# Optimization experiments

Hardware: AMD Instinct MI355X
Metric: run time of the kernel (lower is better)

Reference implementation:

```python
import jax, jax.numpy as jnp
import numpy as np

B, C, D, DE, NH = 4, 4, 96, 96, 3
NS, HIN, TOTAL_Z, PZ = 12, 128, 64, 32
WZ = WH = WW = 4
N_WIN_TOK = WZ * WH * WW  # 64 tokens per 3D window


def _rel_index():
    # standard Swin-3D relative position index, (N, N) into a (7*7*7, NH) table
    c = np.stack(np.meshgrid(np.arange(WZ), np.arange(WH), np.arange(WW), indexing='ij')).reshape(3, -1)
    r = (c[:, :, None] - c[:, None, :]).transpose(1, 2, 0)
    r += np.array([WZ - 1, WH - 1, WW - 1])
    r[:, :, 0] *= (2 * WH - 1) * (2 * WW - 1)
    r[:, :, 1] *= (2 * WW - 1)
    return jnp.asarray(r.sum(-1))

REL_IDX = _rel_index()


def layernorm(x, g, b, eps=1e-5):
    m = x.mean(-1, keepdims=True)
    v = x.var(-1, keepdims=True)
    return (x - m) * jax.lax.rsqrt(v + eps) * g + b


def groupnorm(x, g, b, groups=8, eps=1e-5):
    Bb, Cc, Z, H, W = x.shape
    xr = x.reshape(Bb, groups, Cc // groups, Z, H, W)
    m = xr.mean((2, 3, 4, 5), keepdims=True)
    v = xr.var((2, 3, 4, 5), keepdims=True)
    xr = (xr - m) * jax.lax.rsqrt(v + eps)
    return xr.reshape(Bb, Cc, Z, H, W) * g[None, :, None, None, None] + b[None, :, None, None, None]


def conv3d(x, w, b):
    y = jax.lax.conv_general_dilated(x, w, (1, 1, 1), 'SAME', dimension_numbers=('NCDHW', 'OIDHW', 'NCDHW'))
    return y + b[None, :, None, None, None]


def z_interp(x, pos, out_z):
    """Linear interp along z. x:(B,C,S,H,W), pos:(S,) sorted float positions.
    Matches the torch loop: clamp below first / above last, weight=0.5 on ties."""
    S = x.shape[2]
    zq = jnp.arange(out_z, dtype=jnp.float32)
    right = jnp.searchsorted(pos, zq, side='left')  # first i with pos[i] >= z
    left = jnp.clip(right - 1, 0, S - 1)
    rc = jnp.clip(right, 0, S - 1)
    lp, rp = pos[left], pos[rc]
    d = rp - lp
    w = jnp.where(d > 0, (zq - lp) / jnp.where(d > 0, d, 1.0), 0.5)
    w = w[None, None, :, None, None]
    return (1.0 - w) * x[:, :, left] + w * x[:, :, rc]


def reference(sparse_obs, encoder_feat, pe_w, pe_b, pe_g, pe_beta, enc_w, enc_b, ln_g, ln_b,
              qkv_w, qkv_b, attn_w, attn_b, rpb, ref_w1, ref_b1, gn1_g, gn1_b,
              ref_w2, ref_b2, gn2_g, gn2_b, rec_w, rec_b, sparse_indices):
    Bb, Cc, Sz, H, W = sparse_obs.shape
    pos = sparse_indices.astype(jnp.float32)
    # --- skip connection: z-interp baseline at full resolution ---
    baseline = z_interp(sparse_obs, pos, TOTAL_Z)  # (B,C,64,128,128)
    # --- sparse patch embed: conv (1,4,4) stride (1,4,4) + LN ---
    xr = sparse_obs.reshape(Bb, Cc, Sz, H // 4, 4, W // 4, 4)
    f = jnp.einsum('bczhpwq,dcpq->bdzhw', xr, pe_w) + pe_b[None, :, None, None, None]
    f = layernorm(f.transpose(0, 2, 3, 4, 1), pe_g, pe_beta).transpose(0, 4, 1, 2, 3)
    # position-aware z interpolation into patch space (patch_size_z = 2)
    f = z_interp(f, pos / 2.0, PZ)  # (B,D,32,32,32)
    # --- encoder 1x1x1 projection + fuse ---
    enc = jnp.einsum('bczhw,dc->bdzhw', encoder_feat, enc_w) + enc_b[None, :, None, None, None]
    f = f + enc
    # --- 3D window attention with relative position bias (pre-norm, residual) ---
    nz = PZ // WZ
    x = f.transpose(0, 2, 3, 4, 1)  # (B,Z,H,W,D)
    xw = x.reshape(Bb, nz, WZ, nz, WH, nz, WW, D).transpose(0, 1, 3, 5, 2, 4, 6, 7).reshape(-1, N_WIN_TOK, D)
    sc = xw
    xn = layernorm(xw, ln_g, ln_b)
    dh = D // NH
    qkv = (xn @ qkv_w.T + qkv_b).reshape(-1, N_WIN_TOK, 3, NH, dh).transpose(2, 0, 3, 1, 4)
    q, k, v = qkv[0], qkv[1], qkv[2]  # (nWin*B, NH, N, dh)
    att = jnp.einsum('whnd,whmd->whnm', q * (dh ** -0.5), k)
    att = att + rpb[REL_IDX].transpose(2, 0, 1)[None]  # (.., NH, N, N)
    att = jax.nn.softmax(att, axis=-1)
    o = jnp.einsum('whnm,whmd->whnd', att, v).transpose(0, 2, 1, 3).reshape(-1, N_WIN_TOK, D)
    xw = sc + (o @ attn_w.T + attn_b)
    x = xw.reshape(Bb, nz, nz, nz, WZ, WH, WW, D).transpose(0, 1, 4, 2, 5, 3, 6, 7).reshape(Bb, PZ, PZ, PZ, D)
    f = x.transpose(0, 4, 1, 2, 3)
    f = jax.nn.gelu(groupnorm(conv3d(f, ref_w1, ref_b1), gn1_g, gn1_b), approximate=False)
    f = jax.nn.gelu(groupnorm(conv3d(f, ref_w2, ref_b2), gn2_g, gn2_b), approximate=False)
    # --- patch recovery: ConvTranspose3d kernel=stride=(2,4,4) as einsum+reshape ---
    delta = jnp.einsum('bizhw,iodef->bozdhewf', f, rec_w).reshape(Bb, Cc, PZ * 2, PZ * 4, PZ * 4)
    delta = delta + rec_b[None, :, None, None, None]
    return baseline + delta


def setup_inputs():
    key = jax.random.key(0)
    ks = jax.random.split(key, 16)
    n = lambda i, shape: jax.random.normal(ks[i], shape, dtype=jnp.float32) * 0.02
    return {
        'sparse_obs': jax.random.normal(ks[0], (B, C, NS, HIN, HIN), dtype=jnp.float32),
        'encoder_feat': jax.random.normal(ks[1], (B, DE, PZ, PZ, PZ), dtype=jnp.float32),
        'pe_w': n(2, (D, C, 4, 4)), 'pe_b': jnp.zeros((D,)), 'pe_g': jnp.ones((D,)), 'pe_beta': jnp.zeros((D,)),
        'enc_w': n(3, (D, DE)), 'enc_b': jnp.zeros((D,)),
        'ln_g': jnp.ones((D,)), 'ln_b': jnp.zeros((D,)),
        'qkv_w': n(4, (3 * D, D)), 'qkv_b': jnp.zeros((3 * D,)),
        'attn_w': n(5, (D, D)), 'attn_b': jnp.zeros((D,)),
        'rpb': n(6, ((2 * WZ - 1) * (2 * WH - 1) * (2 * WW - 1), NH)),
        'ref_w1': n(7, (D, D, 3, 3, 3)), 'ref_b1': jnp.zeros((D,)), 'gn1_g': jnp.ones((D,)), 'gn1_b': jnp.zeros((D,)),
        'ref_w2': n(8, (D, D, 3, 3, 3)), 'ref_b2': jnp.zeros((D,)), 'gn2_g': jnp.ones((D,)), 'gn2_b': jnp.zeros((D,)),
        'rec_w': n(9, (D, C, 2, 4, 4)), 'rec_b': jnp.zeros((C,)),
        'sparse_indices': jnp.asarray(np.round(np.linspace(0, 63, 12)).astype(np.int64)),
    }
```

## Files before the change

kernel.cpp:

```cpp
#include <hip/hip_runtime.h>
#include <math.h>

typedef __attribute__((ext_vector_type(8))) short short8v;
typedef __attribute__((ext_vector_type(4))) float float4v;

__device__ inline unsigned short f2bf(float f) {
  unsigned u = __float_as_uint(f);
  return (unsigned short)((u + 0x7fff + ((u >> 16) & 1)) >> 16);
}
__device__ inline unsigned pk2(float a, float b) {
  return (unsigned)f2bf(a) | ((unsigned)f2bf(b) << 16);
}
__device__ inline float bfl(unsigned u) { return __uint_as_float(u << 16); }
__device__ inline float bfh(unsigned u) { return __uint_as_float(u & 0xffff0000u); }
__device__ inline float bfs(short s) { return __uint_as_float(((unsigned)(unsigned short)s) << 16); }

__global__ __launch_bounds__(96) void k_tables(const int* __restrict__ sidx, int* __restrict__ T) {
  __shared__ float pos[12];
  int t = threadIdx.x;
  if (t < 12) pos[t] = (float)sidx[t];
  __syncthreads();
  if (t < 64) {
    float zq = (float)t;
    int r = 0;
    while (r < 12 && pos[r] < zq) r++;
    int l = r - 1; if (l < 0) l = 0; if (l > 11) l = 11;
    int rc = r; if (rc > 11) rc = 11;
    float lp = pos[l], rp = pos[rc], d = rp - lp;
    float w = d > 0.f ? (zq - lp) / d : 0.5f;
    T[t] = l; T[64 + t] = rc; ((float*)T)[128 + t] = w;
  } else {
    int zq = t - 64;
    float zqf = (float)zq;
    int r = 0;
    while (r < 12 && pos[r] * 0.5f < zqf) r++;
    int l = r - 1; if (l < 0) l = 0; if (l > 11) l = 11;
    int rc = r; if (rc > 11) rc = 11;
    float lp = pos[l] * 0.5f, rp = pos[rc] * 0.5f, d = rp - lp;
    float w = d > 0.f ? (zqf - lp) / d : 0.5f;
    T[192 + zq] = l; T[224 + zq] = rc; ((float*)T)[256 + zq] = w;
  }
}

__global__ __launch_bounds__(256) void k_wcv(const float* __restrict__ w, short* __restrict__ Wt) {
  int id = blockIdx.x * 256 + threadIdx.x;
  if (id >= 248832) return;
  float v = w[id];
  int o = id / 2592; int rem = id % 2592; int i = rem / 27; int tap = rem % 27;
  Wt[(tap * 96 + o) * 96 + i] = (short)f2bf(v);
}

__global__ __launch_bounds__(256) void k_cvt(const float* __restrict__ src, short* __restrict__ dst, int n) {
  int id = blockIdx.x * 256 + threadIdx.x;
  if (id < n) dst[id] = (short)f2bf(src[id]);
}

__global__ __launch_bounds__(256) void k_wrt(const float* __restrict__ src, short* __restrict__ dst) {
  int id = blockIdx.x * 256 + threadIdx.x;
  if (id >= 12288) return;
  int i = id >> 7, j = id & 127;
  dst[j * 96 + i] = (short)f2bf(src[id]);
}

__global__ __launch_bounds__(256) void k_bias(const float* __restrict__ rpb, float* __restrict__ Bt) {
  int id = blockIdx.x * 256 + threadIdx.x;
  if (id >= 12288) return;
  int head = id >> 12, rem = id & 4095, n = rem >> 6, m = rem & 63;
  int dz = (n >> 4) - (m >> 4), dh = ((n >> 2) & 3) - ((m >> 2) & 3), dw = (n & 3) - (m & 3);
  Bt[id] = rpb[((dz + 3) * 49 + (dh + 3) * 7 + (dw + 3)) * 3 + head];
}

__global__ __launch_bounds__(256) void k_pe(const float* __restrict__ sp, const short* __restrict__ Wpe,
    const float* __restrict__ pb, const float* __restrict__ pg, const float* __restrict__ pbeta,
    float* __restrict__ f1) {
  int x = blockIdx.x;
  int b = x / 384, z = (x / 32) % 12, h = x % 32;
  __shared__ short sB[32][72];
  __shared__ float sF[32][97];
  __shared__ float sM[32], sR[32];
  int tid = threadIdx.x;
  for (int id = tid; id < 2048; id += 256) {
    int c = id >> 9, p = (id >> 7) & 3, col = id & 127;
    float v = sp[(((b * 4 + c) * 12 + z) * 128 + h * 4 + p) * 128 + col];
    sB[col >> 2][c * 16 + p * 4 + (col & 3)] = (short)f2bf(v);
  }
  __syncthreads();
  int w = tid >> 6, l = tid & 63, lo = l & 15, ig = l >> 4;
  int nt = w & 1, mbase = (w >> 1) * 3;
  short8v bfrag[2];
  #pragma unroll
  for (int kc = 0; kc < 2; kc++)
    bfrag[kc] = *(const short8v*)&sB[nt * 16 + lo][kc * 32 + ig * 8];
  #pragma unroll
  for (int mi = 0; mi < 3; mi++) {
    int m = mbase + mi;
    float4v acc = (float4v){0.f, 0.f, 0.f, 0.f};
    #pragma unroll
    for (int kc = 0; kc < 2; kc++) {
      short8v a = *(const short8v*)(Wpe + (size_t)(m * 16 + lo) * 64 + kc * 32 + ig * 8);
      acc = __builtin_amdgcn_mfma_f32_16x16x32_bf16(a, bfrag[kc], acc, 0, 0, 0);
    }
    int wcoord = nt * 16 + lo;
    #pragma unroll
    for (int r = 0; r < 4; r++) {
      int d = m * 16 + ig * 4 + r;
      sF[wcoord][d] = acc[r] + pb[d];
    }
  }
  __syncthreads();
  if (tid < 32) {
    int wv = tid;
    float s = 0.f, ss = 0.f;
    for (int d = 0; d < 96; d++) { float v = sF[wv][d]; s += v; ss += v * v; }
    float m = s * (1.f / 96.f);
    float var = ss * (1.f / 96.f) - m * m;
    sM[wv] = m; sR[wv] = rsqrtf(var + 1e-5f);
  }
  __syncthreads();
  for (int id = tid; id < 3072; id += 256) {
    int d = id >> 5, wv = id & 31;
    float v = (sF[wv][d] - sM[wv]) * sR[wv] * pg[d] + pbeta[d];
    f1[(((b * 96 + d) * 12 + z) * 32 + h) * 32 + wv] = v;
  }
}

__global__ __launch_bounds__(256) void k_ie(const float* __restrict__ f1, const float* __restrict__ ef,
    const short* __restrict__ Wenc, const float* __restrict__ eb, const int* __restrict__ T,
    unsigned* __restrict__ Xg) {
  int x = blockIdx.x;
  int b = x >> 9, chunk = x & 511;
  int v0 = chunk * 64;
  int z = v0 >> 10, rp = v0 & 1023;
  int zl = T[192 + z], zr = T[224 + z];
  float wt = ((const float*)T)[256 + z];
  __shared__ short sEb[64][104];
  int tid = threadIdx.x;
  for (int id = tid; id < 6144; id += 256) {
    int c = id >> 6, vs = id & 63;
    sEb[vs][c] = (short)f2bf(ef[(size_t)(b * 96 + c) * 32768 + v0 + vs]);
  }
  __syncthreads();
  int w = tid >> 6, l = tid & 63, lo = l & 15, ig = l >> 4;
  int vcol = w * 16 + lo;
  short8v bfrag[3];
  #pragma unroll
  for (int kc = 0; kc < 3; kc++)
    bfrag[kc] = *(const short8v*)&sEb[vcol][kc * 32 + ig * 8];
  float4v acc[6];
  #pragma unroll
  for (int m = 0; m < 6; m++) {
    acc[m] = (float4v){0.f, 0.f, 0.f, 0.f};
    #pragma unroll
    for (int kc = 0; kc < 3; kc++) {
      short8v a = *(const short8v*)(Wenc + (size_t)(m * 16 + lo) * 96 + kc * 32 + ig * 8);
      acc[m] = __builtin_amdgcn_mfma_f32_16x16x32_bf16(a, bfrag[kc], acc[m], 0, 0, 0);
    }
  }
  int zb = z >> 2, tz = z & 3;
  int h0 = (chunk & 15) * 2;
  int h = h0 + (vcol >> 5), wc = vcol & 31;
  int win = ((b * 8 + zb) * 8 + (h >> 2)) * 8 + (wc >> 2);
  int t = tz * 16 + (h & 3) * 4 + (wc & 3);
  size_t xbase = (size_t)(win * 64 + t) * 48;
  float wl = 1.f - wt;
  #pragma unroll
  for (int m = 0; m < 6; m++) {
    #pragma unroll
    for (int rr = 0; rr < 2; rr++) {
      int d0 = m * 16 + ig * 4 + rr * 2;
      const float* p1a = f1 + ((size_t)(b * 96 + d0) * 12 + zl) * 1024 + rp + vcol;
      const float* p2a = f1 + ((size_t)(b * 96 + d0) * 12 + zr) * 1024 + rp + vcol;
      const float* p1b = f1 + ((size_t)(b * 96 + d0 + 1) * 12 + zl) * 1024 + rp + vcol;
      const float* p2b = f1 + ((size_t)(b * 96 + d0 + 1) * 12 + zr) * 1024 + rp + vcol;
      float va = acc[m][rr * 2] + eb[d0] + wl * p1a[0] + wt * p2a[0];
      float vb = acc[m][rr * 2 + 1] + eb[d0 + 1] + wl * p1b[0] + wt * p2b[0];
      Xg[xbase + m * 8 + ig * 2 + rr] = pk2(va, vb);
    }
  }
}

__global__ __launch_bounds__(512) void k_qkv(const unsigned* __restrict__ Xg, const short* __restrict__ Wq,
    const float* __restrict__ qb, const float* __restrict__ lg, const float* __restrict__ lb,
    short* __restrict__ Qg, short* __restrict__ Kg, short* __restrict__ Vg) {
  int win = blockIdx.x;
  __shared__ short sX[64][104];
  __shared__ short sVt[96][72];
  __shared__ float sM[64], sRr[64];
  int tid = threadIdx.x;
  for (int id = tid; id < 3072; id += 512) {
    int row = id / 48, c2 = id % 48;
    *(unsigned*)&sX[row][c2 * 2] = Xg[(size_t)(win * 64 + row) * 48 + c2];
  }
  __syncthreads();
  {
    int token = tid >> 3, j = tid & 7;
    float s = 0.f, ss = 0.f;
    #pragma unroll
    for (int i = 0; i < 12; i++) {
      float v = bfs(sX[token][j * 12 + i]);
      s += v; ss += v * v;
    }
    s += __shfl_xor(s, 1); ss += __shfl_xor(ss, 1);
    s += __shfl_xor(s, 2); ss += __shfl_xor(ss, 2);
    s += __shfl_xor(s, 4); ss += __shfl_xor(ss, 4);
    if (j == 0) {
      float m = s * (1.f / 96.f);
      sM[token] = m;
      sRr[token] = rsqrtf(ss * (1.f / 96.f) - m * m + 1e-5f);
    }
  }
  __syncthreads();
  for (int id = tid; id < 3072; id += 512) {
    int row = id / 48, c2 = id % 48;
    unsigned u = *(unsigned*)&sX[row][c2 * 2];
    float m = sM[row], r = sRr[row];
    float v0 = (bfl(u) - m) * r * lg[2 * c2] + lb[2 * c2];
    float v1 = (bfh(u) - m) * r * lg[2 * c2 + 1] + lb[2 * c2 + 1];
    *(unsigned*)&sX[row][c2 * 2] = pk2(v0, v1);
  }
  __syncthreads();
  int w = tid >> 6, l = tid & 63, lo = l & 15, ig = l >> 4;
  int mt2 = w >> 1, nh = w & 1;
  short8v a[3];
  #pragma unroll
  for (int kc = 0; kc < 3; kc++)
    a[kc] = *(const short8v*)&sX[mt2 * 16 + lo][kc * 32 + ig * 8];
  for (int nt = nh * 9; nt < nh * 9 + 9; nt++) {
    float4v acc = (float4v){0.f, 0.f, 0.f, 0.f};
    #pragma unroll
    for (int kc = 0; kc < 3; kc++) {
      short8v bfr = *(const short8v*)(Wq + (size_t)(nt * 16 + lo) * 96 + kc * 32 + ig * 8);
      acc = __builtin_amdgcn_mfma_f32_16x16x32_bf16(a[kc], bfr, acc, 0, 0, 0);
    }
    int out = nt * 16 + lo;
    float bias = qb[out];
    if (nt < 6) {
      int head = out >> 5, c = out & 31;
      #pragma unroll
      for (int r = 0; r < 4; r++)
        Qg[((size_t)(win * 3 + head) * 64 + mt2 * 16 + ig * 4 + r) * 32 + c] =
            (short)f2bf((acc[r] + bias) * 0.17677669529663687f);
    } else if (nt < 12) {
      int o2 = out - 96, head = o2 >> 5, c = o2 & 31;
      #pragma unroll
      for (int r = 0; r < 4; r++)
        Kg[((size_t)(win * 3 + head) * 64 + mt2 * 16 + ig * 4 + r) * 32 + c] = (short)f2bf(acc[r] + bias);
    } else {
      int o2 = out - 192;
      #pragma unroll
      for (int r = 0; r < 4; r++)
        sVt[o2][mt2 * 16 + ig * 4 + r] = (short)f2bf(acc[r] + bias);
    }
  }
  __syncthreads();
  for (int id = tid; id < 768; id += 512) {
    int row = id >> 3, ch = id & 7;
    short8v v = *(short8v*)&sVt[row][ch * 8];
    *(short8v*)(Vg + ((size_t)(win * 3 + (row >> 5)) * 32 + (row & 31)) * 64 + ch * 8) = v;
  }
}

__global__ __launch_bounds__(256) void k_att2(const short* __restrict__ Qg, const short* __restrict__ Kg,
    const short* __restrict__ Vg, const float* __restrict__ Bt, short* __restrict__ Og) {
  __shared__ short Pl[4][64][72];
  int tid = threadIdx.x;
  int w = tid >> 6, l = tid & 63, lo = l & 15, ig = l >> 4;
  int gwh = blockIdx.x * 4 + w;
  int head = gwh % 3, win = gwh / 3;
  short8v q[4], k[4];
  #pragma unroll
  for (int mt = 0; mt < 4; mt++)
    q[mt] = *(const short8v*)(Qg + ((size_t)gwh * 64 + mt * 16 + lo) * 32 + ig * 8);
  #pragma unroll
  for (int nt = 0; nt < 4; nt++)
    k[nt] = *(const short8v*)(Kg + ((size_t)gwh * 64 + nt * 16 + lo) * 32 + ig * 8);
  float4v s[4][4];
  #pragma unroll
  for (int mt = 0; mt < 4; mt++)
    #pragma unroll
    for (int nt = 0; nt < 4; nt++)
      s[mt][nt] = __builtin_amdgcn_mfma_f32_16x16x32_bf16(q[mt], k[nt], (float4v){0.f, 0.f, 0.f, 0.f}, 0, 0, 0);
  const float* bt = Bt + head * 4096;
  #pragma unroll
  for (int mt = 0; mt < 4; mt++) {
    #pragma unroll
    for (int r = 0; r < 4; r++) {
      int tok = mt * 16 + ig * 4 + r;
      float v[4];
      float mx = -1e30f;
      #pragma unroll
      for (int nt = 0; nt < 4; nt++) {
        v[nt] = s[mt][nt][r] + bt[tok * 64 + nt * 16 + lo];
        mx = fmaxf(mx, v[nt]);
      }
      mx = fmaxf(mx, __shfl_xor(mx, 1));
      mx = fmaxf(mx, __shfl_xor(mx, 2));
      mx = fmaxf(mx, __shfl_xor(mx, 4));
      mx = fmaxf(mx, __shfl_xor(mx, 8));
      float sm = 0.f;
      #pragma unroll
      for (int nt = 0; nt < 4; nt++) { v[nt] = __expf(v[nt] - mx); sm += v[nt]; }
      sm += __shfl_xor(sm, 1);
      sm += __shfl_xor(sm, 2);
      sm += __shfl_xor(sm, 4);
      sm += __shfl_xor(sm, 8);
      float inv = 1.f / sm;
      #pragma unroll
      for (int nt = 0; nt < 4; nt++)
        Pl[w][tok][nt * 16 + lo] = (short)f2bf(v[nt] * inv);
    }
  }
  short8v pa[4][2], vb[2][2];
  #pragma unroll
  for (int mt = 0; mt < 4; mt++)
    #pragma unroll
    for (int kc = 0; kc < 2; kc++)
      pa[mt][kc] = *(const short8v*)&Pl[w][mt * 16 + lo][kc * 32 + ig * 8];
  #pragma unroll
  for (int ct = 0; ct < 2; ct++)
    #pragma unroll
    for (int kc = 0; kc < 2; kc++)
      vb[ct][kc] = *(const short8v*)(Vg + ((size_t)gwh * 32 + ct * 16 + lo) * 64 + kc * 32 + ig * 8);
  #pragma unroll
  for (int mt = 0; mt < 4; mt++)
    #pragma unroll
    for (int ct = 0; ct < 2; ct++) {
      float4v o = __builtin_amdgcn_mfma_f32_16x16x32_bf16(pa[mt][0], vb[ct][0], (float4v){0.f, 0.f, 0.f, 0.f}, 0, 0, 0);
      o = __builtin_amdgcn_mfma_f32_16x16x32_bf16(pa[mt][1], vb[ct][1], o, 0, 0, 0);
      #pragma unroll
      for (int r = 0; r < 4; r++)
        Og[((size_t)(win * 64 + mt * 16 + ig * 4 + r)) * 96 + head * 32 + ct * 16 + lo] = (short)f2bf(o[r]);
    }
}

__global__ __launch_bounds__(256) void k_proj(const short* __restrict__ Og, const unsigned* __restrict__ Xg,
    const short* __restrict__ Wa, const float* __restrict__ ab, short* __restrict__ Xt) {
  int win = blockIdx.x;
  __shared__ float sOut[64][100];
  int tid = threadIdx.x;
  int w = tid >> 6, l = tid & 63, lo = l & 15, ig = l >> 4;
  int mt = w;
  short8v a[3];
  #pragma unroll
  for (int kc = 0; kc < 3; kc++)
    a[kc] = *(const short8v*)(Og + ((size_t)(win * 64 + mt * 16 + lo)) * 96 + kc * 32 + ig * 8);
  #pragma unroll
  for (int nt = 0; nt < 6; nt++) {
    float4v acc = (float4v){0.f, 0.f, 0.f, 0.f};
    #pragma unroll
    for (int kc = 0; kc < 3; kc++) {
      short8v bfr = *(const short8v*)(Wa + (size_t)(nt * 16 + lo) * 96 + kc * 32 + ig * 8);
      acc = __builtin_amdgcn_mfma_f32_16x16x32_bf16(a[kc], bfr, acc, 0, 0, 0);
    }
    int out = nt * 16 + lo;
    float bias = ab[out];
    #pragma unroll
    for (int r = 0; r < 4; r++) {
      int tok = mt * 16 + ig * 4 + r;
      unsigned u = Xg[(size_t)(win * 64 + tok) * 48 + (out >> 1)];
      sOut[tok][out] = acc[r] + bias + ((out & 1) ? bfh(u) : bfl(u));
    }
  }
  __syncthreads();
  int b = win >> 9, zb = (win >> 6) & 7, hb = (win >> 3) & 7, wb = win & 7;
  for (int id = tid; id < 3072; id += 256) {
    int cc = id >> 10, rem = id & 1023, t = rem >> 4, ilp = rem & 15;
    int d0 = cc * 32 + ilp * 2;
    unsigned pk = pk2(sOut[t][d0], sOut[t][d0 + 1]);
    int tz = t >> 4, th = (t >> 2) & 3, tw = t & 3;
    size_t vox = (size_t)(zb * 4 + tz) * 1024 + (hb * 4 + th) * 32 + wb * 4 + tw;
    ((unsigned*)Xt)[((size_t)(b * 3 + cc) * 32768 + vox) * 16 + ilp] = pk;
  }
}

__global__ __launch_bounds__(512) void k_convM(const short* __restrict__ Xt,
    const short* __restrict__ Wt, const float* __restrict__ cb, float* __restrict__ y,
    float* __restrict__ stats) {
  int x = blockIdx.x;
  int b = x >> 6, zp = (x >> 2) & 15, hq = x & 3;
  int tid = threadIdx.x;
  int wvi = tid >> 6, l = tid & 63;
  int lo = l & 15, ig = l >> 4;
  int hp = wvi & 3, mh = wvi >> 2;
  __shared__ short Xl[54400];
  __shared__ float sG[16];
  if (tid < 16) sG[tid] = 0.f;
  float4v acc[3][2][2][2];
  #pragma unroll
  for (int mi = 0; mi < 3; mi++)
    #pragma unroll
    for (int zo = 0; zo < 2; zo++)
      #pragma unroll
      for (int hr = 0; hr < 2; hr++)
        #pragma unroll
        for (int n = 0; n < 2; n++) acc[mi][zo][hr][n] = (float4v){0.f, 0.f, 0.f, 0.f};

  for (int c = 0; c < 3; c++) {
    __syncthreads();
    for (int r = 0; r < 11; r++) {
      int id = tid + 512 * r;
      if (id < 5440) {
        int seg = id & 3, q = id >> 2;
        int zz = q / 340, rem = q - zz * 340;
        int hh = rem / 34, ww = rem - hh * 34;
        int gz = zp * 2 + zz - 1, gh = hq * 8 + hh - 1, gw = ww - 1;
        int4 val = {0, 0, 0, 0};
        if (gz >= 0 && gz < 32 && gh >= 0 && gh < 32 && gw >= 0 && gw < 32)
          val = *(const int4*)(Xt + ((size_t)((b * 3 + c) * 32768 + (gz << 10) + (gh << 5) + gw) * 32 + seg * 8));
        *(int4*)(&Xl[q * 40 + seg * 8]) = val;
      }
    }
    __syncthreads();
    for (int dh = 0; dh < 3; dh++) {
      for (int dwv = 0; dwv < 3; dwv++) {
        short8v bfr[4][2][2];
        #pragma unroll
        for (int zr = 0; zr < 4; zr++)
          #pragma unroll
          for (int hr = 0; hr < 2; hr++)
            #pragma unroll
            for (int n = 0; n < 2; n++) {
              int vox = (zr * 10 + hp * 2 + hr + dh) * 34 + n * 16 + lo + dwv;
              bfr[zr][hr][n] = *(const short8v*)&Xl[vox * 40 + ig * 8];
            }
        #pragma unroll
        for (int dz = 0; dz < 3; dz++) {
          int tap = dz * 9 + dh * 3 + dwv;
          #pragma unroll
          for (int mi = 0; mi < 3; mi++) {
            short8v wf = *(const short8v*)(Wt +
                ((size_t)(tap * 96 + (mh * 3 + mi) * 16 + lo)) * 96 + c * 32 + ig * 8);
            #pragma unroll
            for (int zo = 0; zo < 2; zo++)
              #pragma unroll
              for (int hr = 0; hr < 2; hr++)
                #pragma unroll
                for (int n = 0; n < 2; n++)
                  acc[mi][zo][hr][n] = __builtin_amdgcn_mfma_f32_16x16x32_bf16(wf, bfr[zo + dz][hr][n], acc[mi][zo][hr][n], 0, 0, 0);
          }
        }
      }
    }
  }
  #pragma unroll
  for (int mi = 0; mi < 3; mi++) {
    #pragma unroll
    for (int r = 0; r < 4; r++) {
      int o = (mh * 3 + mi) * 16 + ig * 4 + r;
      float cbo = cb[o];
      float s = 0.f, ss = 0.f;
      #pragma unroll
      for (int zo = 0; zo < 2; zo++)
        #pragma unroll
        for (int hr = 0; hr < 2; hr++)
          #pragma unroll
          for (int n = 0; n < 2; n++) {
            float v = acc[mi][zo][hr][n][r] + cbo;
            int z = zp * 2 + zo;
            int h = hq * 8 + hp * 2 + hr;
            int vcol = n * 16 + lo;
            y[((size_t)(b * 96 + o) << 15) + (z << 10) + (h << 5) + vcol] = v;
            s += v; ss += v * v;
          }
      s += __shfl_xor(s, 1); ss += __shfl_xor(ss, 1);
      s += __shfl_xor(s, 2); ss += __shfl_xor(ss, 2);
      s += __shfl_xor(s, 4); ss += __shfl_xor(ss, 4);
      s += __shfl_xor(s, 8); ss += __shfl_xor(ss, 8);
      if (lo == 0) {
        int gl = o / 12;
        atomicAdd(&sG[gl * 2], s);
        atomicAdd(&sG[gl * 2 + 1], ss);
      }
    }
  }
  __syncthreads();
  if (tid < 16) atomicAdd(&stats[b * 16 + tid], sG[tid]);
}

__global__ __launch_bounds__(256) void k_gn(const float* __restrict__ y, const float* __restrict__ stats,
    const float* __restrict__ gg, const float* __restrict__ gb, short* __restrict__ xt) {
  int x = blockIdx.x;
  int b = x / 1536, r = x % 1536, c = r / 512, vt = r % 512;
  int v0 = vt * 64;
  __shared__ float sT[64][33];
  int tid = threadIdx.x;
  const float invN = 1.f / 393216.f;
  for (int id = tid; id < 512; id += 256) {
    int ol = id >> 4, vq = id & 15;
    int o = c * 32 + ol, g = b * 8 + o / 12;
    float m = stats[2 * g] * invN;
    float var = stats[2 * g + 1] * invN - m * m;
    float rs = rsqrtf(var + 1e-5f) * gg[o];
    float bb = gb[o];
    float4 v = *(const float4*)&y[((size_t)(b * 96 + o) << 15) + v0 + vq * 4];
    float vv[4] = {v.x, v.y, v.z, v.w};
    #pragma unroll
    for (int j = 0; j < 4; j++) {
      float val = (vv[j] - m) * rs + bb;
      sT[vq * 4 + j][ol] = 0.5f * val * (1.f + erff(val * 0.70710678118654752f));
    }
  }
  __syncthreads();
  for (int id = tid; id < 1024; id += 256) {
    int v = id >> 4, p = id & 15;
    ((unsigned*)xt)[((size_t)(b * 3 + c) * 32768 + v0 + v) * 16 + p] = pk2(sT[v][2 * p], sT[v][2 * p + 1]);
  }
}

__global__ __launch_bounds__(256) void k_final(const short* __restrict__ f5b, const float* __restrict__ sp,
    const short* __restrict__ Wrec, const float* __restrict__ rb, const int* __restrict__ T,
    float* __restrict__ out) {
  int x = blockIdx.x;
  int b = x >> 10, chunk = x & 1023;
  int z = chunk >> 5, h = chunk & 31;
  int v0 = chunk * 32;
  int tid = threadIdx.x;
  int w = tid >> 6, l = tid & 63, lo = l & 15, ig = l >> 4;
  short8v afrag[2][3];
  #pragma unroll
  for (int mt = 0; mt < 2; mt++)
    #pragma unroll
    for (int kc = 0; kc < 3; kc++)
      afrag[mt][kc] = *(const short8v*)(f5b +
          ((size_t)(b * 3 + kc) * 32768 + v0 + mt * 16 + lo) * 32 + ig * 8);
  float4v acc[2][2];
  #pragma unroll
  for (int nt2 = 0; nt2 < 2; nt2++) {
    int jt = w * 2 + nt2;
    #pragma unroll
    for (int mt = 0; mt < 2; mt++) acc[mt][nt2] = (float4v){0.f, 0.f, 0.f, 0.f};
    #pragma unroll
    for (int kc = 0; kc < 3; kc++) {
      short8v bfr = *(const short8v*)(Wrec + (size_t)(jt * 16 + lo) * 96 + kc * 32 + ig * 8);
      #pragma unroll
      for (int mt = 0; mt < 2; mt++)
        acc[mt][nt2] = __builtin_amdgcn_mfma_f32_16x16x32_bf16(afrag[mt][kc], bfr, acc[mt][nt2], 0, 0, 0);
    }
  }
  const float* w64 = (const float*)(T + 128);
  #pragma unroll
  for (int mt = 0; mt < 2; mt++)
    #pragma unroll
    for (int nt2 = 0; nt2 < 2; nt2++) {
      int jt = w * 2 + nt2;
      #pragma unroll
      for (int r = 0; r < 4; r++) {
        int wv = mt * 16 + ig * 4 + r;
        int j = jt * 16 + lo;
        int o = j >> 5, dd = (j >> 4) & 1, e = (j >> 2) & 3, ff = j & 3;
        int Z = 2 * z + dd, H = 4 * h + e, W = 4 * wv + ff;
        int zl = T[Z], zr = T[64 + Z];
        float bw = w64[Z];
        const float* spb = sp + (size_t)(b * 4 + o) * 196608;
        float bval = (1.f - bw) * spb[(size_t)zl * 16384 + H * 128 + W]
                   + bw * spb[(size_t)zr * 16384 + H * 128 + W];
        out[((size_t)(b * 4 + o) * 64 + Z) * 16384 + H * 128 + W] = bval + acc[mt][nt2][r] + rb[o];
      }
    }
}

extern "C" void kernel_launch(void* const* d_in, const int* in_sizes, int n_in,
                              void* d_out, int out_size, void* d_ws, size_t ws_size,
                              hipStream_t stream) {
  const float* sp    = (const float*)d_in[0];
  const float* ef    = (const float*)d_in[1];
  const float* pe_w  = (const float*)d_in[2];
  const float* pe_b  = (const float*)d_in[3];
  const float* pe_g  = (const float*)d_in[4];
  const float* pe_be = (const float*)d_in[5];
  const float* enc_w = (const float*)d_in[6];
  const float* enc_b = (const float*)d_in[7];
  const float* ln_g  = (const float*)d_in[8];
  const float* ln_b  = (const float*)d_in[9];
  const float* qkv_w = (const float*)d_in[10];
  const float* qkv_b = (const float*)d_in[11];
  const float* at_w  = (const float*)d_in[12];
  const float* at_b  = (const float*)d_in[13];
  const float* rpb   = (const float*)d_in[14];
  const float* w1    = (const float*)d_in[15];
  const float* b1    = (const float*)d_in[16];
  const float* g1g   = (const float*)d_in[17];
  const float* g1b   = (const float*)d_in[18];
  const float* w2    = (const float*)d_in[19];
  const float* b2    = (const float*)d_in[20];
  const float* g2g   = (const float*)d_in[21];
  const float* g2b   = (const float*)d_in[22];
  const float* recw  = (const float*)d_in[23];
  const float* recb  = (const float*)d_in[24];
  const int*   sidx  = (const int*)d_in[25];
  float* out = (float*)d_out;

  char* ws = (char*)d_ws;
  unsigned* Xg = (unsigned*)ws;
  float* f1    = (float*)(ws + 25165824);
  short* Qg    = (short*)(ws + 25165824);
  short* Kg    = (short*)(ws + 50331648);
  short* Vg    = (short*)(ws + 75497472);
  short* XtA   = (short*)(ws + 25165824);
  float* Y     = (float*)(ws + 50331648);
  int*   T     = (int*)(ws + 100663296);
  float* stats = (float*)(ws + 100665344);
  short* Wrec  = (short*)(ws + 100666368);

  char* dob = (char*)d_out;
  short* Og   = (short*)d_out;
  short* Wenc = (short*)(dob + 25165824);
  short* Wpe  = (short*)(dob + 25184256);
  short* Wqkv = (short*)(dob + 65937408);
  short* Waw  = (short*)(dob + 65992704);
  float* Bt   = (float*)(dob + 66011136);
  short* Wt1  = (short*)(dob + 66060288);
  short* Wt2  = (short*)(dob + 66557952);

  k_tables<<<1, 96, 0, stream>>>(sidx, T);
  k_wcv<<<972, 256, 0, stream>>>(w1, Wt1);
  k_wcv<<<972, 256, 0, stream>>>(w2, Wt2);
  k_cvt<<<108, 256, 0, stream>>>(qkv_w, Wqkv, 27648);
  k_cvt<<<36, 256, 0, stream>>>(at_w, Waw, 9216);
  k_cvt<<<36, 256, 0, stream>>>(enc_w, Wenc, 9216);
  k_cvt<<<24, 256, 0, stream>>>(pe_w, Wpe, 6144);
  k_wrt<<<48, 256, 0, stream>>>(recw, Wrec);
  k_bias<<<48, 256, 0, stream>>>(rpb, Bt);

  k_pe<<<1536, 256, 0, stream>>>(sp, Wpe, pe_b, pe_g, pe_be, f1);
  k_ie<<<2048, 256, 0, stream>>>(f1, ef, Wenc, enc_b, T, Xg);
  k_qkv<<<2048, 512, 0, stream>>>(Xg, Wqkv, qkv_b, ln_g, ln_b, Qg, Kg, Vg);
  k_att2<<<1536, 256, 0, stream>>>(Qg, Kg, Vg, Bt, Og);
  k_proj<<<2048, 256, 0, stream>>>(Og, Xg, Waw, at_b, XtA);

  hipMemsetAsync(stats, 0, 64 * sizeof(float), stream);
  k_convM<<<256, 512, 0, stream>>>(XtA, Wt1, b1, Y, stats);
  k_gn<<<6144, 256, 0, stream>>>(Y, stats, g1g, g1b, XtA);

  hipMemsetAsync(stats, 0, 64 * sizeof(float), stream);
  k_convM<<<256, 512, 0, stream>>>(XtA, Wt2, b2, Y, stats);
  k_gn<<<6144, 256, 0, stream>>>(Y, stats, g2g, g2b, XtA);

  k_final<<<4096, 256, 0, stream>>>(XtA, sp, Wrec, recb, T, out);
}
```

Measured before the change: 370.1 us.

## Shrink conv tiles, XOR-swizzle LDS, and store conv output as bf16

The 3D conv kernel now runs 512 blocks of 256 threads, each covering half the H range, with a smaller LDS halo tile. The tile uses an XOR swizzle instead of 40-short padding to avoid bank conflicts. The pre-groupnorm activation is written as bf16 instead of fp32, halving that intermediate's write and read traffic, and the GN kernel reads 8 bf16 values per thread. Costs are more halo reloading per output and bf16 rounding of the intermediate before normalization (statistics still come from fp32).

```diff
diff --git a/kernel.cpp b/kernel.cpp
--- a/kernel.cpp
+++ b/kernel.cpp
@@ -373,16 +373,16 @@
   }
 }
 
-__global__ __launch_bounds__(512) void k_convM(const short* __restrict__ Xt,
-    const short* __restrict__ Wt, const float* __restrict__ cb, float* __restrict__ y,
+__global__ __launch_bounds__(256) void k_convM(const short* __restrict__ Xt,
+    const short* __restrict__ Wt, const float* __restrict__ cb, short* __restrict__ y16,
     float* __restrict__ stats) {
   int x = blockIdx.x;
-  int b = x >> 6, zp = (x >> 2) & 15, hq = x & 3;
+  int b = x >> 7, zp = (x >> 3) & 15, hq = x & 7;
   int tid = threadIdx.x;
   int wvi = tid >> 6, l = tid & 63;
   int lo = l & 15, ig = l >> 4;
-  int hp = wvi & 3, mh = wvi >> 2;
-  __shared__ short Xl[54400];
+  int hp = wvi & 1, mh = wvi >> 1;
+  __shared__ short Xl[816 * 32];
   __shared__ float sG[16];
   if (tid < 16) sG[tid] = 0.f;
   float4v acc[3][2][2][2];
@@ -397,17 +397,18 @@
 
   for (int c = 0; c < 3; c++) {
     __syncthreads();
-    for (int r = 0; r < 11; r++) {
-      int id = tid + 512 * r;
-      if (id < 5440) {
+    for (int r = 0; r < 13; r++) {
+      int id = tid + 256 * r;
+      if (id < 3264) {
         int seg = id & 3, q = id >> 2;
-        int zz = q / 340, rem = q - zz * 340;
+        int zz = q / 204, rem = q - zz * 204;
         int hh = rem / 34, ww = rem - hh * 34;
-        int gz = zp * 2 + zz - 1, gh = hq * 8 + hh - 1, gw = ww - 1;
+        int gz = zp * 2 + zz - 1, gh = hq * 4 + hh - 1, gw = ww - 1;
         int4 val = {0, 0, 0, 0};
         if (gz >= 0 && gz < 32 && gh >= 0 && gh < 32 && gw >= 0 && gw < 32)
           val = *(const int4*)(Xt + ((size_t)((b * 3 + c) * 32768 + (gz << 10) + (gh << 5) + gw) * 32 + seg * 8));
-        *(int4*)(&Xl[q * 40 + seg * 8]) = val;
+        int slot = seg ^ ((q >> 1) & 3);
+        *(int4*)(&Xl[q * 32 + slot * 8]) = val;
       }
     }
     __syncthreads();
@@ -420,8 +421,8 @@
           for (int hr = 0; hr < 2; hr++)
             #pragma unroll
             for (int n = 0; n < 2; n++) {
-              int vox = (zr * 10 + hp * 2 + hr + dh) * 34 + n * 16 + lo + dwv;
-              bfr[zr][hr][n] = *(const short8v*)&Xl[vox * 40 + ig * 8];
+              int vox = (zr * 6 + hp * 2 + hr + dh) * 34 + n * 16 + lo + dwv;
+              bfr[zr][hr][n] = *(const short8v*)&Xl[vox * 32 + ((ig ^ ((vox >> 1) & 3)) * 8)];
             }
         #pragma unroll
         for (int dz = 0; dz < 3; dz++) {
@@ -457,9 +458,9 @@
           for (int n = 0; n < 2; n++) {
             float v = acc[mi][zo][hr][n][r] + cbo;
             int z = zp * 2 + zo;
-            int h = hq * 8 + hp * 2 + hr;
+            int h = hq * 4 + hp * 2 + hr;
             int vcol = n * 16 + lo;
-            y[((size_t)(b * 96 + o) << 15) + (z << 10) + (h << 5) + vcol] = v;
+            y16[((size_t)(b * 96 + o) << 15) + (z << 10) + (h << 5) + vcol] = (short)f2bf(v);
             s += v; ss += v * v;
           }
       s += __shfl_xor(s, 1); ss += __shfl_xor(ss, 1);
@@ -477,7 +478,7 @@
   if (tid < 16) atomicAdd(&stats[b * 16 + tid], sG[tid]);
 }
 
-__global__ __launch_bounds__(256) void k_gn(const float* __restrict__ y, const float* __restrict__ stats,
+__global__ __launch_bounds__(256) void k_gn(const short* __restrict__ y16, const float* __restrict__ stats,
     const float* __restrict__ gg, const float* __restrict__ gb, short* __restrict__ xt) {
   int x = blockIdx.x;
   int b = x / 1536, r = x % 1536, c = r / 512, vt = r % 512;
@@ -485,19 +486,18 @@
   __shared__ float sT[64][33];
   int tid = threadIdx.x;
   const float invN = 1.f / 393216.f;
-  for (int id = tid; id < 512; id += 256) {
-    int ol = id >> 4, vq = id & 15;
+  {
+    int ol = tid >> 3, vq = tid & 7;
     int o = c * 32 + ol, g = b * 8 + o / 12;
     float m = stats[2 * g] * invN;
     float var = stats[2 * g + 1] * invN - m * m;
     float rs = rsqrtf(var + 1e-5f) * gg[o];
     float bb = gb[o];
-    float4 v = *(const float4*)&y[((size_t)(b * 96 + o) << 15) + v0 + vq * 4];
-    float vv[4] = {v.x, v.y, v.z, v.w};
-    #pragma unroll
-    for (int j = 0; j < 4; j++) {
-      float val = (vv[j] - m) * rs + bb;
-      sT[vq * 4 + j][ol] = 0.5f * val * (1.f + erff(val * 0.70710678118654752f));
+    short8v yv = *(const short8v*)&y16[((size_t)(b * 96 + o) << 15) + v0 + vq * 8];
+    #pragma unroll
+    for (int j = 0; j < 8; j++) {
+      float val = (bfs(yv[j]) - m) * rs + bb;
+      sT[vq * 8 + j][ol] = 0.5f * val * (1.f + erff(val * 0.70710678118654752f));
     }
   }
   __syncthreads();
@@ -597,7 +597,7 @@
   short* Kg    = (short*)(ws + 50331648);
   short* Vg    = (short*)(ws + 75497472);
   short* XtA   = (short*)(ws + 25165824);
-  float* Y     = (float*)(ws + 50331648);
+  short* Y16   = (short*)(ws + 50331648);
   int*   T     = (int*)(ws + 100663296);
   float* stats = (float*)(ws + 100665344);
   short* Wrec  = (short*)(ws + 100666368);
@@ -629,12 +629,12 @@
   k_proj<<<2048, 256, 0, stream>>>(Og, Xg, Waw, at_b, XtA);
 
   hipMemsetAsync(stats, 0, 64 * sizeof(float), stream);
-  k_convM<<<256, 512, 0, stream>>>(XtA, Wt1, b1, Y, stats);
-  k_gn<<<6144, 256, 0, stream>>>(Y, stats, g1g, g1b, XtA);
+  k_convM<<<512, 256, 0, stream>>>(XtA, Wt1, b1, Y16, stats);
+  k_gn<<<6144, 256, 0, stream>>>(Y16, stats, g1g, g1b, XtA);
 
   hipMemsetAsync(stats, 0, 64 * sizeof(float), stream);
-  k_convM<<<256, 512, 0, stream>>>(XtA, Wt2, b2, Y, stats);
-  k_gn<<<6144, 256, 0, stream>>>(Y, stats, g2g, g2b, XtA);
+  k_convM<<<512, 256, 0, stream>>>(XtA, Wt2, b2, Y16, stats);
+  k_gn<<<6144, 256, 0, stream>>>(Y16, stats, g2g, g2b, XtA);
 
   k_final<<<4096, 256, 0, stream>>>(XtA, sp, Wrec, recb, T, out);
 }
```

Result: faster. 357.4 us (-3.4%).
